# Kernel optimization log

Hardware: AMD Instinct MI355X
Metric: run time of the kernel (lower is better)

The kernel has to match this reference:

```python
import jax, jax.numpy as jnp
import numpy as np

B, H, L, D = 16, 8, 128, 64
SCALE = jnp.float32(np.sqrt(D))
NEG = jnp.float32(-1e9)


def setup_inputs() -> dict:
    key = jax.random.key(0)
    kq, kk, kv, km = jax.random.split(key, 4)
    Q = jax.random.normal(kq, (B, H, L, D), dtype=jnp.float32)
    K = jax.random.normal(kk, (H, B, L, D), dtype=jnp.float32)
    V = jax.random.normal(kv, (H, B, L, D), dtype=jnp.float32)
    mask = jax.random.randint(km, (B, 1, 1, L, L), 0, 2, dtype=jnp.int32)
    return {"Q": Q, "K": K, "V": V, "mask": mask}


def reference(Q, K, V, mask):
    # Cross-sample (intersample) attention:
    # scores[b,h,c,i,j] = <Q[b,h,i,:], K[h,c,j,:]> / sqrt(D)  -> (B,H,B,L,L)
    scores = jnp.einsum('bhid,hcjd->bhcij', Q, K) / SCALE
    scores = jnp.where(mask == 0, NEG, scores)
    attn_weights = jax.nn.softmax(scores, axis=-1)  # (B,H,B,L,L)
    # output[b,h,c,i,:] = sum_j w[b,h,c,i,j] * V[h,c,j,:]  -> (B,H,B,L,D)
    output = jnp.einsum('bhcij,hcjd->bhcid', attn_weights, V)
    return (output, attn_weights)
```

## Files before the change

kernel.cpp:

```cpp
#include <hip/hip_runtime.h>
#include <hip/hip_bf16.h>

typedef float  f32x4  __attribute__((ext_vector_type(4)));
typedef __bf16 bf16x8 __attribute__((ext_vector_type(8)));

#define MFMA16(A,B,C) __builtin_amdgcn_mfma_f32_16x16x32_bf16((A),(B),(C),0,0,0)

constexpr int BN = 16, HN = 8, LN = 128, DN = 64;
constexpr size_t OUT0 = (size_t)BN * HN * BN * LN * DN;

constexpr int QE = BN * HN * LN * DN;
constexpr size_t MBOFF = 4 * (size_t)QE;
constexpr size_t WS_BYTES = (MBOFF + (size_t)BN * LN * LN) * sizeof(__bf16);

constexpr int PS  = 36;
constexpr int KTS = 72;
constexpr int VTS = 136;


__device__ __forceinline__ void load8_split(const float* __restrict__ p, float scale,
                                            bf16x8& hi, bf16x8& lo) {
  float f[8];
  *(float4*)&f[0] = *(const float4*)(p);
  *(float4*)&f[4] = *(const float4*)(p + 4);
#pragma unroll
  for (int i = 0; i < 8; ++i) {
    float x = f[i] * scale;
    __bf16 h = (__bf16)x;
    hi[i] = h;
    lo[i] = (__bf16)(x - (float)h);
  }
}

__device__ __forceinline__ void lds8_split(const float* p, bf16x8& hi, bf16x8& lo) {
  float f[8];
  *(float4*)&f[0] = *(const float4*)(p);
  *(float4*)&f[4] = *(const float4*)(p + 4);
#pragma unroll
  for (int i = 0; i < 8; ++i) {
    __bf16 h = (__bf16)f[i];
    hi[i] = h;
    lo[i] = (__bf16)(f[i] - (float)h);
  }
}

__device__ __forceinline__ void gload_lds16(const void* g, void* l) {
  __builtin_amdgcn_global_load_lds(
      (const __attribute__((address_space(1))) unsigned int*)g,
      (__attribute__((address_space(3))) unsigned int*)l, 16, 0, 0);
}

__device__ __forceinline__ f32x4 ntld4(const float* p) {
  return __builtin_nontemporal_load((const f32x4*)p);
}
__device__ __forceinline__ void ntst4(float* p, f32x4 v) {
  __builtin_nontemporal_store(v, (f32x4*)p);
}

__global__ __launch_bounds__(256) void pre_kernel(
    const float* __restrict__ Q, const float* __restrict__ K,
    const float* __restrict__ V, const int* __restrict__ M,
    __bf16* __restrict__ ws)
{
  const int t   = threadIdx.x;
  const int blk = blockIdx.x;

  if (blk < 512) {
    int base = blk * 2048 + t * 8;
    float f[8];
    *(f32x4*)&f[0] = ntld4(Q + base);
    *(f32x4*)&f[4] = ntld4(Q + base + 4);
    bf16x8 hi, lo;
#pragma unroll
    for (int i = 0; i < 8; ++i) {
      float x = f[i] * 0.125f;
      __bf16 h = (__bf16)x;
      hi[i] = h;
      lo[i] = (__bf16)(x - (float)h);
    }
    *(bf16x8*)&ws[base]      = hi;
    *(bf16x8*)&ws[QE + base] = lo;
  } else if (blk < 1024) {
    int g  = (blk - 512) * 256 + t;
    int k0 = (g & 7) * 8;
    int n  = (g >> 3) & 127;
    int hc = g >> 10;
    const float* src = K + ((size_t)hc * LN + n) * DN + k0;
    float f[8];
    *(f32x4*)&f[0] = ntld4(src);
    *(f32x4*)&f[4] = ntld4(src + 4);
    bf16x8 kk;
#pragma unroll
    for (int i = 0; i < 8; ++i) kk[i] = (__bf16)f[i];
    int k0s = k0 ^ ((n & 7) << 3);
    *(bf16x8*)&ws[2 * (size_t)QE + (size_t)hc * 8192 + n * 64 + k0s] = kk;
  } else if (blk < 1152) {
    int hc = blk - 1024;
    int j8 = t >> 4;
    int d0 = (t & 15) * 4;
    const float* Vp = V + (size_t)hc * (LN * DN);
    f32x4 vv[8];
#pragma unroll
    for (int r = 0; r < 8; ++r)
      vv[r] = ntld4(Vp + (j8 * 8 + r) * DN + d0);
#pragma unroll
    for (int dw = 0; dw < 4; ++dw) {
      int d = d0 + dw;
      bf16x8 col;
#pragma unroll
      for (int r = 0; r < 8; ++r)
        col[r] = (__bf16)vv[r][dw];
      int js = (j8 * 8) ^ ((d & 7) << 3);
      *(bf16x8*)&ws[3 * (size_t)QE + (size_t)hc * 8192 + d * 128 + js] = col;
    }
  } else {
    int bsel = blk - 1152;
    const int* src = M + (size_t)bsel * (LN * LN);
    __bf16*    dst = ws + MBOFF + (size_t)bsel * (LN * LN);
    int row  = t >> 1;
    int half = t & 1;
#pragma unroll
    for (int g = 0; g < 8; ++g) {
      int l16 = half * 8 + g;
      bf16x8 m8;
#pragma unroll
      for (int ct = 0; ct < 8; ++ct)
        m8[ct] = (__bf16)(float)src[row * LN + ct * 16 + l16];
      *(bf16x8*)&dst[row * LN + l16 * 8] = m8;
    }
  }
}

__global__ __launch_bounds__(256, 3) void isa_attn_fast(
    const __bf16* __restrict__ ws, float* __restrict__ out)
{
  __shared__ __bf16 KT[LN * DN];
  __shared__ __bf16 VT[DN * LN];
  __shared__ float  P [LN * PS];

  const int bid = blockIdx.x;
  const int w = (bid & 7) * 256 + (bid >> 3);
  const int h = w >> 8;
  const int c = (w >> 4) & 15;
  const int b = w & 15;
  const int hc = h * BN + c;

  const __bf16* Qh = ws + (size_t)(b * HN + h) * (LN * DN);
  const __bf16* Ql = Qh + QE;
  const __bf16* Ks = ws + 2 * (size_t)QE + (size_t)hc * 8192;
  const __bf16* Vs = ws + 3 * (size_t)QE + (size_t)hc * 8192;
  const __bf16* Mb = ws + MBOFF + (size_t)b * (LN * LN);
  float* Op = out + (size_t)((b * HN + h) * BN + c) * (LN * DN);
  float* Wp = out + OUT0 + (size_t)((b * HN + h) * BN + c) * (LN * LN);

  const int t    = threadIdx.x;
  const int lane = t & 63;
  const int wid  = t >> 6;
  const int quad = lane >> 4;
  const int l16  = lane & 15;
  const int row0 = wid * 32;
  const int swz  = (l16 & 7) << 3;

  {
    const char* kg = (const char*)Ks;
    const char* vg = (const char*)Vs;
    char* kl = (char*)KT;
    char* vl = (char*)VT;
#pragma unroll
    for (int i = 0; i < 4; ++i)
      gload_lds16(kg + t * 16 + i * 4096, kl + t * 16 + i * 4096);
#pragma unroll
    for (int i = 0; i < 4; ++i)
      gload_lds16(vg + t * 16 + i * 4096, vl + t * 16 + i * 4096);
  }

  bf16x8 qhi[2][2], qlo[2][2];
#pragma unroll
  for (int rt = 0; rt < 2; ++rt)
#pragma unroll
    for (int kt = 0; kt < 2; ++kt) {
      const int off = (row0 + rt * 16 + l16) * DN + kt * 32 + quad * 8;
      qhi[rt][kt] = *(const bf16x8*)(Qh + off);
      qlo[rt][kt] = *(const bf16x8*)(Ql + off);
    }

  __syncthreads();

  f32x4 acc[2][8];
#pragma unroll
  for (int rt = 0; rt < 2; ++rt)
#pragma unroll
    for (int ct = 0; ct < 8; ++ct)
      acc[rt][ct] = (f32x4){0.f, 0.f, 0.f, 0.f};

#pragma unroll
  for (int ct = 0; ct < 8; ++ct) {
#pragma unroll
    for (int kt = 0; kt < 2; ++kt) {
      bf16x8 kh = *(const bf16x8*)&KT[(ct * 16 + l16) * 64 + ((kt * 32 + quad * 8) ^ swz)];
#pragma unroll
      for (int rt = 0; rt < 2; ++rt) {
        acc[rt][ct] = MFMA16(qhi[rt][kt], kh, acc[rt][ct]);
        acc[rt][ct] = MFMA16(qlo[rt][kt], kh, acc[rt][ct]);
      }
    }
  }

#pragma unroll
  for (int rt = 0; rt < 2; ++rt) {
    bf16x8 m8[4];
#pragma unroll
    for (int r = 0; r < 4; ++r) {
      int row = row0 + rt * 16 + quad * 4 + r;
      m8[r] = *(const bf16x8*)&Mb[row * LN + l16 * 8];
    }
#pragma unroll
    for (int r = 0; r < 4; ++r) {
      float mx = -3.0e38f;
#pragma unroll
      for (int ct = 0; ct < 8; ++ct) mx = fmaxf(mx, acc[rt][ct][r]);
      mx = fmaxf(mx, __shfl_xor(mx, 1));
      mx = fmaxf(mx, __shfl_xor(mx, 2));
      mx = fmaxf(mx, __shfl_xor(mx, 4));
      mx = fmaxf(mx, __shfl_xor(mx, 8));
      float s[8];
      float sum = 0.f;
#pragma unroll
      for (int ct = 0; ct < 8; ++ct) {
        s[ct] = __expf(acc[rt][ct][r] - mx) * (float)m8[r][ct];
        sum += s[ct];
      }
      sum += __shfl_xor(sum, 1);
      sum += __shfl_xor(sum, 2);
      sum += __shfl_xor(sum, 4);
      sum += __shfl_xor(sum, 8);
      float inv = __builtin_amdgcn_rcpf(sum);
      inv = inv * (2.0f - sum * inv);
#pragma unroll
      for (int ct = 0; ct < 8; ++ct) acc[rt][ct][r] = s[ct] * inv;
    }
  }

  f32x4 oacc[2][4];
#pragma unroll
  for (int rt = 0; rt < 2; ++rt)
#pragma unroll
    for (int nt = 0; nt < 4; ++nt)
      oacc[rt][nt] = (f32x4){0.f, 0.f, 0.f, 0.f};

#pragma unroll
  for (int qu = 0; qu < 4; ++qu) {
#pragma unroll
    for (int rt = 0; rt < 2; ++rt)
#pragma unroll
      for (int cc = 0; cc < 2; ++cc)
#pragma unroll
        for (int r = 0; r < 4; ++r)
          P[(row0 + rt * 16 + quad * 4 + r) * PS + cc * 16 + l16] =
              acc[rt][qu * 2 + cc][r];

#pragma unroll
    for (int e = 0; e < 4; ++e) {
      int idx = e * 64 + lane;
      int rl  = idx >> 3;
      int c4  = idx & 7;
      f32x4 v = *(const f32x4*)&P[(row0 + rl) * PS + c4 * 4];
      ntst4(&Wp[(size_t)(row0 + rl) * LN + qu * 32 + c4 * 4], v);
    }

    bf16x8 phi[2], plo[2];
#pragma unroll
    for (int rt = 0; rt < 2; ++rt)
      lds8_split(&P[(row0 + rt * 16 + l16) * PS + quad * 8], phi[rt], plo[rt]);
#pragma unroll
    for (int nt = 0; nt < 4; ++nt) {
      bf16x8 vh = *(const bf16x8*)&VT[(nt * 16 + l16) * 128 + ((qu * 32 + quad * 8) ^ swz)];
#pragma unroll
      for (int rt = 0; rt < 2; ++rt) {
        oacc[rt][nt] = MFMA16(phi[rt], vh, oacc[rt][nt]);
        oacc[rt][nt] = MFMA16(plo[rt], vh, oacc[rt][nt]);
      }
    }
  }

#pragma unroll
  for (int hf = 0; hf < 2; ++hf) {
#pragma unroll
    for (int rt = 0; rt < 2; ++rt)
#pragma unroll
      for (int nn = 0; nn < 2; ++nn)
#pragma unroll
        for (int r = 0; r < 4; ++r)
          P[(row0 + rt * 16 + quad * 4 + r) * PS + nn * 16 + l16] =
              oacc[rt][hf * 2 + nn][r];
#pragma unroll
    for (int e = 0; e < 4; ++e) {
      int idx = e * 64 + lane;
      int rl  = idx >> 3;
      int c4  = idx & 7;
      f32x4 v = *(const f32x4*)&P[(row0 + rl) * PS + c4 * 4];
      ntst4(&Op[(size_t)(row0 + rl) * DN + hf * 32 + c4 * 4], v);
    }
  }
}

__global__ __launch_bounds__(256, 3) void isa_attn_kernel(
    const float* __restrict__ Q, const float* __restrict__ K,
    const float* __restrict__ V, const int* __restrict__ M,
    float* __restrict__ out)
{
  __shared__ __bf16 KT[LN * KTS];
  __shared__ __bf16 VT[DN * VTS];
  __shared__ float  P [LN * PS];

  const int bid = blockIdx.x;
  const int w = (bid & 7) * 256 + (bid >> 3);
  const int h = w >> 8;
  const int c = (w >> 4) & 15;
  const int b = w & 15;

  const float* Qp = Q + (size_t)(b * HN + h) * (LN * DN);
  const float* Kp = K + (size_t)(h * BN + c) * (LN * DN);
  const float* Vp = V + (size_t)(h * BN + c) * (LN * DN);
  const int*   Mp = M + (size_t)b * (LN * LN);
  float* Op = out + (size_t)((b * HN + h) * BN + c) * (LN * DN);
  float* Wp = out + OUT0 + (size_t)((b * HN + h) * BN + c) * (LN * LN);

  const int t    = threadIdx.x;
  const int lane = t & 63;
  const int wid  = t >> 6;
  const int quad = lane >> 4;
  const int l16  = lane & 15;
  const int row0 = wid * 32;

#pragma unroll
  for (int it = 0; it < 4; ++it) {
    int idx = t + it * 256;
    int n  = idx >> 3;
    int k0 = (idx & 7) * 8;
    float4 a0 = *(const float4*)(Kp + n * DN + k0);
    float4 a1 = *(const float4*)(Kp + n * DN + k0 + 4);
    bf16x8 kk;
    kk[0] = (__bf16)a0.x; kk[1] = (__bf16)a0.y; kk[2] = (__bf16)a0.z; kk[3] = (__bf16)a0.w;
    kk[4] = (__bf16)a1.x; kk[5] = (__bf16)a1.y; kk[6] = (__bf16)a1.z; kk[7] = (__bf16)a1.w;
    *(bf16x8*)&KT[n * KTS + k0] = kk;
  }

  {
    int j8 = t >> 4;
    int d0 = (t & 15) * 4;
    float4 vv[8];
#pragma unroll
    for (int r = 0; r < 8; ++r)
      vv[r] = *(const float4*)(Vp + (j8 * 8 + r) * DN + d0);
#pragma unroll
    for (int dw = 0; dw < 4; ++dw) {
      bf16x8 col;
#pragma unroll
      for (int r = 0; r < 8; ++r)
        col[r] = (__bf16)(((const float*)&vv[r])[dw]);
      *(bf16x8*)&VT[(d0 + dw) * VTS + j8 * 8] = col;
    }
  }

  bf16x8 qhi[2][2], qlo[2][2];
#pragma unroll
  for (int rt = 0; rt < 2; ++rt)
#pragma unroll
    for (int kt = 0; kt < 2; ++kt)
      load8_split(Qp + (row0 + rt * 16 + l16) * DN + kt * 32 + quad * 8, 0.125f,
                  qhi[rt][kt], qlo[rt][kt]);

  __syncthreads();

  f32x4 acc[2][8];
#pragma unroll
  for (int rt = 0; rt < 2; ++rt)
#pragma unroll
    for (int ct = 0; ct < 8; ++ct)
      acc[rt][ct] = (f32x4){0.f, 0.f, 0.f, 0.f};

#pragma unroll
  for (int ct = 0; ct < 8; ++ct) {
#pragma unroll
    for (int kt = 0; kt < 2; ++kt) {
      bf16x8 kh = *(const bf16x8*)&KT[(ct * 16 + l16) * KTS + kt * 32 + quad * 8];
#pragma unroll
      for (int rt = 0; rt < 2; ++rt) {
        acc[rt][ct] = MFMA16(qhi[rt][kt], kh, acc[rt][ct]);
        acc[rt][ct] = MFMA16(qlo[rt][kt], kh, acc[rt][ct]);
      }
    }
  }

#pragma unroll
  for (int rt = 0; rt < 2; ++rt) {
#pragma unroll
    for (int r = 0; r < 4; ++r) {
      int row = row0 + rt * 16 + quad * 4 + r;
      const int* mrow = Mp + (size_t)row * LN + l16;
      float mf[8];
#pragma unroll
      for (int ct = 0; ct < 8; ++ct) mf[ct] = (float)mrow[ct * 16];
      float mx = -3.0e38f;
#pragma unroll
      for (int ct = 0; ct < 8; ++ct) mx = fmaxf(mx, acc[rt][ct][r]);
      mx = fmaxf(mx, __shfl_xor(mx, 1));
      mx = fmaxf(mx, __shfl_xor(mx, 2));
      mx = fmaxf(mx, __shfl_xor(mx, 4));
      mx = fmaxf(mx, __shfl_xor(mx, 8));
      float s[8];
      float sum = 0.f;
#pragma unroll
      for (int ct = 0; ct < 8; ++ct) {
        s[ct] = __expf(acc[rt][ct][r] - mx) * mf[ct];
        sum += s[ct];
      }
      sum += __shfl_xor(sum, 1);
      sum += __shfl_xor(sum, 2);
      sum += __shfl_xor(sum, 4);
      sum += __shfl_xor(sum, 8);
      float inv = __builtin_amdgcn_rcpf(sum);
      inv = inv * (2.0f - sum * inv);
#pragma unroll
      for (int ct = 0; ct < 8; ++ct) acc[rt][ct][r] = s[ct] * inv;
    }
  }

  f32x4 oacc[2][4];
#pragma unroll
  for (int rt = 0; rt < 2; ++rt)
#pragma unroll
    for (int nt = 0; nt < 4; ++nt)
      oacc[rt][nt] = (f32x4){0.f, 0.f, 0.f, 0.f};

#pragma unroll
  for (int qu = 0; qu < 4; ++qu) {
#pragma unroll
    for (int rt = 0; rt < 2; ++rt)
#pragma unroll
      for (int cc = 0; cc < 2; ++cc)
#pragma unroll
        for (int r = 0; r < 4; ++r)
          P[(row0 + rt * 16 + quad * 4 + r) * PS + cc * 16 + l16] =
              acc[rt][qu * 2 + cc][r];

#pragma unroll
    for (int e = 0; e < 4; ++e) {
      int idx = e * 64 + lane;
      int rl  = idx >> 3;
      int c4  = idx & 7;
      float4 v = *(const float4*)&P[(row0 + rl) * PS + c4 * 4];
      *(float4*)&Wp[(size_t)(row0 + rl) * LN + qu * 32 + c4 * 4] = v;
    }

    bf16x8 phi[2], plo[2];
#pragma unroll
    for (int rt = 0; rt < 2; ++rt)
      lds8_split(&P[(row0 + rt * 16 + l16) * PS + quad * 8], phi[rt], plo[rt]);
#pragma unroll
    for (int nt = 0; nt < 4; ++nt) {
      bf16x8 vh = *(const bf16x8*)&VT[(nt * 16 + l16) * VTS + qu * 32 + quad * 8];
#pragma unroll
      for (int rt = 0; rt < 2; ++rt) {
        oacc[rt][nt] = MFMA16(phi[rt], vh, oacc[rt][nt]);
        oacc[rt][nt] = MFMA16(plo[rt], vh, oacc[rt][nt]);
      }
    }
  }

#pragma unroll
  for (int hf = 0; hf < 2; ++hf) {
#pragma unroll
    for (int rt = 0; rt < 2; ++rt)
#pragma unroll
      for (int nn = 0; nn < 2; ++nn)
#pragma unroll
        for (int r = 0; r < 4; ++r)
          P[(row0 + rt * 16 + quad * 4 + r) * PS + nn * 16 + l16] =
              oacc[rt][hf * 2 + nn][r];
#pragma unroll
    for (int e = 0; e < 4; ++e) {
      int idx = e * 64 + lane;
      int rl  = idx >> 3;
      int c4  = idx & 7;
      float4 v = *(const float4*)&P[(row0 + rl) * PS + c4 * 4];
      *(float4*)&Op[(size_t)(row0 + rl) * DN + hf * 32 + c4 * 4] = v;
    }
  }
}

extern "C" void kernel_launch(void* const* d_in, const int* in_sizes, int n_in,
                              void* d_out, int out_size, void* d_ws, size_t ws_size,
                              hipStream_t stream) {
  const float* Q = (const float*)d_in[0];
  const float* K = (const float*)d_in[1];
  const float* V = (const float*)d_in[2];
  const int*   M = (const int*)d_in[3];
  if (d_ws != nullptr && ws_size >= WS_BYTES) {
    __bf16* ws = (__bf16*)d_ws;
    pre_kernel<<<dim3(1168), dim3(256), 0, stream>>>(Q, K, V, M, ws);
    isa_attn_fast<<<dim3(BN * HN * BN), dim3(256), 0, stream>>>(ws, (float*)d_out);
  } else {
    isa_attn_kernel<<<dim3(BN * HN * BN), dim3(256), 0, stream>>>(Q, K, V, M, (float*)d_out);
  }
}
```

Before: 228.2 us.

## Use 512-thread blocks with one 16-row tile per wave and DPP reductions

Doubles the threads per block of the main attention kernel from 4 to 8 waves, so each wave handles a single 16-row tile instead of two. This halves per-wave register and accumulator state and spreads the K/V LDS fill and output stores over more threads. It also replaces the shuffle-based 16-lane max/sum reductions with DPP row operations. The cost is more waves competing for LDS and scheduling, and less reuse of each loaded K/V fragment per wave.

```diff
diff --git a/kernel.cpp b/kernel.cpp
--- a/kernel.cpp
+++ b/kernel.cpp
@@ -5,6 +5,20 @@
 typedef __bf16 bf16x8 __attribute__((ext_vector_type(8)));
 
 #define MFMA16(A,B,C) __builtin_amdgcn_mfma_f32_16x16x32_bf16((A),(B),(C),0,0,0)
+
+#define DPPI(x, ctrl) __int_as_float(__builtin_amdgcn_mov_dpp(__float_as_int(x), (ctrl), 0xF, 0xF, true))
+#define DPP_MAX16(x) do { \
+  x = fmaxf(x, DPPI(x, 0x140));  \
+  x = fmaxf(x, DPPI(x, 0x141));  \
+  x = fmaxf(x, DPPI(x, 0x1B));   \
+  x = fmaxf(x, DPPI(x, 0xB1));   \
+} while (0)
+#define DPP_SUM16(x) do { \
+  x += DPPI(x, 0x140); \
+  x += DPPI(x, 0x141); \
+  x += DPPI(x, 0x1B);  \
+  x += DPPI(x, 0xB1);  \
+} while (0)
 
 constexpr int BN = 16, HN = 8, LN = 128, DN = 64;
 constexpr size_t OUT0 = (size_t)BN * HN * BN * LN * DN;
@@ -131,7 +145,7 @@
   }
 }
 
-__global__ __launch_bounds__(256, 3) void isa_attn_fast(
+__global__ __launch_bounds__(512, 4) void isa_attn_fast(
     const __bf16* __restrict__ ws, float* __restrict__ out)
 {
   __shared__ __bf16 KT[LN * DN];
@@ -158,7 +172,7 @@
   const int wid  = t >> 6;
   const int quad = lane >> 4;
   const int l16  = lane & 15;
-  const int row0 = wid * 32;
+  const int row0 = wid * 16;
   const int swz  = (l16 & 7) << 3;
 
   {
@@ -167,100 +181,81 @@
     char* kl = (char*)KT;
     char* vl = (char*)VT;
 #pragma unroll
-    for (int i = 0; i < 4; ++i)
-      gload_lds16(kg + t * 16 + i * 4096, kl + t * 16 + i * 4096);
-#pragma unroll
-    for (int i = 0; i < 4; ++i)
-      gload_lds16(vg + t * 16 + i * 4096, vl + t * 16 + i * 4096);
-  }
-
-  bf16x8 qhi[2][2], qlo[2][2];
-#pragma unroll
-  for (int rt = 0; rt < 2; ++rt)
-#pragma unroll
-    for (int kt = 0; kt < 2; ++kt) {
-      const int off = (row0 + rt * 16 + l16) * DN + kt * 32 + quad * 8;
-      qhi[rt][kt] = *(const bf16x8*)(Qh + off);
-      qlo[rt][kt] = *(const bf16x8*)(Ql + off);
-    }
+    for (int i = 0; i < 2; ++i)
+      gload_lds16(kg + t * 16 + i * 8192, kl + t * 16 + i * 8192);
+#pragma unroll
+    for (int i = 0; i < 2; ++i)
+      gload_lds16(vg + t * 16 + i * 8192, vl + t * 16 + i * 8192);
+  }
+
+  bf16x8 qhi[2], qlo[2];
+#pragma unroll
+  for (int kt = 0; kt < 2; ++kt) {
+    const int off = (row0 + l16) * DN + kt * 32 + quad * 8;
+    qhi[kt] = *(const bf16x8*)(Qh + off);
+    qlo[kt] = *(const bf16x8*)(Ql + off);
+  }
 
   __syncthreads();
 
-  f32x4 acc[2][8];
-#pragma unroll
-  for (int rt = 0; rt < 2; ++rt)
-#pragma unroll
-    for (int ct = 0; ct < 8; ++ct)
-      acc[rt][ct] = (f32x4){0.f, 0.f, 0.f, 0.f};
+  f32x4 acc[8];
+#pragma unroll
+  for (int ct = 0; ct < 8; ++ct)
+    acc[ct] = (f32x4){0.f, 0.f, 0.f, 0.f};
 
 #pragma unroll
   for (int ct = 0; ct < 8; ++ct) {
 #pragma unroll
     for (int kt = 0; kt < 2; ++kt) {
       bf16x8 kh = *(const bf16x8*)&KT[(ct * 16 + l16) * 64 + ((kt * 32 + quad * 8) ^ swz)];
-#pragma unroll
-      for (int rt = 0; rt < 2; ++rt) {
-        acc[rt][ct] = MFMA16(qhi[rt][kt], kh, acc[rt][ct]);
-        acc[rt][ct] = MFMA16(qlo[rt][kt], kh, acc[rt][ct]);
-      }
-    }
-  }
-
-#pragma unroll
-  for (int rt = 0; rt < 2; ++rt) {
+      acc[ct] = MFMA16(qhi[kt], kh, acc[ct]);
+      acc[ct] = MFMA16(qlo[kt], kh, acc[ct]);
+    }
+  }
+
+  {
     bf16x8 m8[4];
 #pragma unroll
     for (int r = 0; r < 4; ++r) {
-      int row = row0 + rt * 16 + quad * 4 + r;
+      int row = row0 + quad * 4 + r;
       m8[r] = *(const bf16x8*)&Mb[row * LN + l16 * 8];
     }
 #pragma unroll
     for (int r = 0; r < 4; ++r) {
       float mx = -3.0e38f;
 #pragma unroll
-      for (int ct = 0; ct < 8; ++ct) mx = fmaxf(mx, acc[rt][ct][r]);
-      mx = fmaxf(mx, __shfl_xor(mx, 1));
-      mx = fmaxf(mx, __shfl_xor(mx, 2));
-      mx = fmaxf(mx, __shfl_xor(mx, 4));
-      mx = fmaxf(mx, __shfl_xor(mx, 8));
+      for (int ct = 0; ct < 8; ++ct) mx = fmaxf(mx, acc[ct][r]);
+      DPP_MAX16(mx);
       float s[8];
       float sum = 0.f;
 #pragma unroll
       for (int ct = 0; ct < 8; ++ct) {
-        s[ct] = __expf(acc[rt][ct][r] - mx) * (float)m8[r][ct];
+        s[ct] = __expf(acc[ct][r] - mx) * (float)m8[r][ct];
         sum += s[ct];
       }
-      sum += __shfl_xor(sum, 1);
-      sum += __shfl_xor(sum, 2);
-      sum += __shfl_xor(sum, 4);
-      sum += __shfl_xor(sum, 8);
+      DPP_SUM16(sum);
       float inv = __builtin_amdgcn_rcpf(sum);
       inv = inv * (2.0f - sum * inv);
 #pragma unroll
-      for (int ct = 0; ct < 8; ++ct) acc[rt][ct][r] = s[ct] * inv;
-    }
-  }
-
-  f32x4 oacc[2][4];
-#pragma unroll
-  for (int rt = 0; rt < 2; ++rt)
-#pragma unroll
-    for (int nt = 0; nt < 4; ++nt)
-      oacc[rt][nt] = (f32x4){0.f, 0.f, 0.f, 0.f};
+      for (int ct = 0; ct < 8; ++ct) acc[ct][r] = s[ct] * inv;
+    }
+  }
+
+  f32x4 oacc[4];
+#pragma unroll
+  for (int nt = 0; nt < 4; ++nt)
+    oacc[nt] = (f32x4){0.f, 0.f, 0.f, 0.f};
 
 #pragma unroll
   for (int qu = 0; qu < 4; ++qu) {
 #pragma unroll
-    for (int rt = 0; rt < 2; ++rt)
-#pragma unroll
-      for (int cc = 0; cc < 2; ++cc)
-#pragma unroll
-        for (int r = 0; r < 4; ++r)
-          P[(row0 + rt * 16 + quad * 4 + r) * PS + cc * 16 + l16] =
-              acc[rt][qu * 2 + cc][r];
-
-#pragma unroll
-    for (int e = 0; e < 4; ++e) {
+    for (int cc = 0; cc < 2; ++cc)
+#pragma unroll
+      for (int r = 0; r < 4; ++r)
+        P[(row0 + quad * 4 + r) * PS + cc * 16 + l16] = acc[qu * 2 + cc][r];
+
+#pragma unroll
+    for (int e = 0; e < 2; ++e) {
       int idx = e * 64 + lane;
       int rl  = idx >> 3;
       int c4  = idx & 7;
@@ -268,33 +263,25 @@
       ntst4(&Wp[(size_t)(row0 + rl) * LN + qu * 32 + c4 * 4], v);
     }
 
-    bf16x8 phi[2], plo[2];
-#pragma unroll
-    for (int rt = 0; rt < 2; ++rt)
-      lds8_split(&P[(row0 + rt * 16 + l16) * PS + quad * 8], phi[rt], plo[rt]);
+    bf16x8 phi, plo;
+    lds8_split(&P[(row0 + l16) * PS + quad * 8], phi, plo);
 #pragma unroll
     for (int nt = 0; nt < 4; ++nt) {
       bf16x8 vh = *(const bf16x8*)&VT[(nt * 16 + l16) * 128 + ((qu * 32 + quad * 8) ^ swz)];
-#pragma unroll
-      for (int rt = 0; rt < 2; ++rt) {
-        oacc[rt][nt] = MFMA16(phi[rt], vh, oacc[rt][nt]);
-        oacc[rt][nt] = MFMA16(plo[rt], vh, oacc[rt][nt]);
-      }
+      oacc[nt] = MFMA16(phi, vh, oacc[nt]);
+      oacc[nt] = MFMA16(plo, vh, oacc[nt]);
     }
   }
 
 #pragma unroll
   for (int hf = 0; hf < 2; ++hf) {
 #pragma unroll
-    for (int rt = 0; rt < 2; ++rt)
-#pragma unroll
-      for (int nn = 0; nn < 2; ++nn)
-#pragma unroll
-        for (int r = 0; r < 4; ++r)
-          P[(row0 + rt * 16 + quad * 4 + r) * PS + nn * 16 + l16] =
-              oacc[rt][hf * 2 + nn][r];
-#pragma unroll
-    for (int e = 0; e < 4; ++e) {
+    for (int nn = 0; nn < 2; ++nn)
+#pragma unroll
+      for (int r = 0; r < 4; ++r)
+        P[(row0 + quad * 4 + r) * PS + nn * 16 + l16] = oacc[hf * 2 + nn][r];
+#pragma unroll
+    for (int e = 0; e < 2; ++e) {
       int idx = e * 64 + lane;
       int rl  = idx >> 3;
       int c4  = idx & 7;
@@ -500,7 +487,7 @@
   if (d_ws != nullptr && ws_size >= WS_BYTES) {
     __bf16* ws = (__bf16*)d_ws;
     pre_kernel<<<dim3(1168), dim3(256), 0, stream>>>(Q, K, V, M, ws);
-    isa_attn_fast<<<dim3(BN * HN * BN), dim3(256), 0, stream>>>(ws, (float*)d_out);
+    isa_attn_fast<<<dim3(BN * HN * BN), dim3(512), 0, stream>>>(ws, (float*)d_out);
   } else {
     isa_attn_kernel<<<dim3(BN * HN * BN), dim3(256), 0, stream>>>(Q, K, V, M, (float*)d_out);
   }
```

After: 222.5 us. -2.5%, faster.
